# Optimization experiments

Hardware: AMD Instinct MI355X
Metric: run time of the kernel (lower is better)

## Reference

```python
import jax, jax.numpy as jnp
import numpy as np

B, N = 4, 512
D_MODEL, ATOM_CH = 256, 5
PAIR_H, N_RBF, RBF_MAX = 128, 16, 4.0
LN_EPS = 1e-5


def setup_inputs() -> dict:
    key = jax.random.key(0)
    ks = jax.random.split(key, 12)
    sd = 1.0 / np.sqrt(D_MODEL)
    sh = 1.0 / np.sqrt(PAIR_H)
    return {
        "trunk_out": jax.random.normal(ks[0], (B, N, D_MODEL), jnp.float32),
        "coords": jax.random.normal(ks[1], (B, N, 3), jnp.float32),
        "pad_mask": jax.random.randint(ks[2], (B, N), 0, 2).astype(bool),
        "ln_g": jnp.ones((D_MODEL,), jnp.float32),
        "ln_b": jnp.zeros((D_MODEL,), jnp.float32),
        "w_a1": jax.random.normal(ks[3], (D_MODEL, D_MODEL), jnp.float32) * sd,
        "b_a1": jnp.zeros((D_MODEL,), jnp.float32),
        "w_a2": jax.random.normal(ks[4], (D_MODEL, ATOM_CH), jnp.float32) * sd,
        "b_a2": jnp.zeros((ATOM_CH,), jnp.float32),
        "w_pi": jax.random.normal(ks[5], (D_MODEL, PAIR_H), jnp.float32) * sd,
        "w_pj": jax.random.normal(ks[6], (D_MODEL, PAIR_H), jnp.float32) * sd,
        "w_pr": jax.random.normal(ks[7], (N_RBF, PAIR_H), jnp.float32) * 0.25,
        "b_p1": jnp.zeros((PAIR_H,), jnp.float32),
        "w_p2": jax.random.normal(ks[8], (PAIR_H,), jnp.float32) * sh,
        "b_p2": jnp.zeros((1,), jnp.float32),
    }


def _forward(trunk_out, coords, pad_mask, ln_g, ln_b, w_a1, b_a1, w_a2, b_a2,
             w_pi, w_pj, w_pr, b_p1, w_p2, b_p2):
    dt = trunk_out.dtype
    valid = ~pad_mask                                   # (B, N)
    validf = valid.astype(dt)

    # ---- atom head: LayerNorm -> Linear -> SiLU -> Linear, pad-masked ----
    mu = trunk_out.mean(-1, keepdims=True)
    var = jnp.mean((trunk_out - mu) ** 2, -1, keepdims=True)
    xn = (trunk_out - mu) * jax.lax.rsqrt(var + LN_EPS) * ln_g + ln_b
    atom_delta = jax.nn.silu(xn @ w_a1 + b_a1) @ w_a2 + b_a2
    atom_delta = jnp.where(pad_mask[..., None], jnp.zeros((), dt), atom_delta)

    # ---- geometry features (non-periodic adapter) ----
    delta = coords[:, :, None, :] - coords[:, None, :, :]   # (B, N, N, 3)
    sq = jnp.sum(delta * delta, -1)
    dist = jnp.sqrt(jnp.maximum(sq, 1e-12))                 # safe sqrt (diag)
    centers = jnp.linspace(0.0, RBF_MAX, N_RBF, dtype=dt)
    gamma = jnp.asarray(1.0 / (RBF_MAX / max(N_RBF - 1, 1)) ** 2, dt)
    rbf = jnp.exp(-gamma * (dist[..., None] - centers) ** 2)  # (B, N, N, R)
    pair_mask = valid[:, :, None] & valid[:, None, :]

    # ---- pair head: LazyLinear on cat([hi, hj, rbf]) == sum of 3 projections ----
    pi = jnp.einsum('bid,dh->bih', trunk_out, w_pi)         # (B, N, H)
    pj = jnp.einsum('bjd,dh->bjh', trunk_out, w_pj)
    h1 = jax.nn.silu(pi[:, :, None, :] + pj[:, None, :, :]
                     + jnp.einsum('bijr,rh->bijh', rbf, w_pr) + b_p1)
    pw = jnp.einsum('bijh,h->bij', h1, w_p2) + b_p2[0]      # (B, N, N)
    pw = jnp.where(pair_mask, pw, jnp.zeros((), dt))
    pw = jnp.where(jnp.eye(N, dtype=bool), jnp.zeros((), dt), pw)  # zero diag

    # ---- weighted-sum coordinate update ----
    coord_delta = jnp.einsum('bij,bijc->bic', pw, delta)    # (B, N, 3)
    denom = jnp.maximum(validf.sum(1, keepdims=True), 1.0)  # (B, 1)
    coord_delta = coord_delta / denom[..., None]
    coord_delta = jnp.where(pad_mask[..., None], jnp.zeros((), dt), coord_delta)
    mean = (coord_delta * validf[..., None]).sum(1, keepdims=True) / denom[..., None]
    coord_delta = jnp.where(pad_mask[..., None], jnp.zeros((), dt), coord_delta - mean)
    return atom_delta, coord_delta


def reference(trunk_out, coords, pad_mask, ln_g, ln_b, w_a1, b_a1, w_a2, b_a2,
              w_pi, w_pj, w_pr, b_p1, w_p2, b_p2):
    return _forward(trunk_out, coords, pad_mask, ln_g, ln_b, w_a1, b_a1,
                    w_a2, b_a2, w_pi, w_pj, w_pr, b_p1, w_p2, b_p2)
```

## Files before the change

kernel.cpp:

```cpp
#include <hip/hip_runtime.h>
#include <hip/hip_bf16.h>

#define BN 2048
#define NSEQ 512
#define D 256
#define H 128
#define R 16
#define AC 5
#define CHUNK 128
#define ROWG 4
#define SPLIT 4

using bf16 = __hip_bfloat16;

__device__ __forceinline__ float fast_silu(float t) {
    const float e = __expf(-t);
    return t * __builtin_amdgcn_rcpf(1.0f + e);
}
__device__ __forceinline__ float bf2f(unsigned short u) {
    return __uint_as_float(((unsigned)u) << 16);
}

__global__ __launch_bounds__(256) void batch_kernel(
    const int* __restrict__ pad, int* __restrict__ jlist_g, int* __restrict__ M_g)
{
    const int b = blockIdx.x;
    const int tid = threadIdx.x;
    __shared__ int s_wcnt[8];
    __shared__ int s_wbase[8];
    const int wv = tid >> 6, lane = tid & 63;
    unsigned long long bm[2];
    #pragma unroll
    for (int cc = 0; cc < 2; ++cc) {
        const int j = cc * 256 + tid;
        const int ok = (pad[b * NSEQ + j] == 0);
        bm[cc] = __ballot(ok);
        if (lane == 0) s_wcnt[cc * 4 + wv] = __popcll(bm[cc]);
    }
    __syncthreads();
    if (tid == 0) {
        int acc = 0;
        #pragma unroll
        for (int q = 0; q < 8; ++q) { s_wbase[q] = acc; acc += s_wcnt[q]; }
        M_g[b] = acc;
    }
    __syncthreads();
    #pragma unroll
    for (int cc = 0; cc < 2; ++cc) {
        const int j = cc * 256 + tid;
        if (pad[b * NSEQ + j] == 0) {
            const int pos = s_wbase[cc * 4 + wv]
                          + __popcll(bm[cc] & ((1ull << lane) - 1ull));
            jlist_g[b * NSEQ + pos] = j;
        }
    }
}

__global__ __launch_bounds__(256) void row_kernel(
    const float* __restrict__ trunk, const int* __restrict__ pad,
    const float* __restrict__ ln_g, const float* __restrict__ ln_b,
    const float* __restrict__ w_a1, const float* __restrict__ b_a1,
    const float* __restrict__ w_a2, const float* __restrict__ b_a2,
    const float* __restrict__ w_pi, const float* __restrict__ w_pj,
    const float* __restrict__ b_p1,
    float* __restrict__ out_atom, float* __restrict__ pj_o,
    unsigned short* __restrict__ pib_o)
{
    const int row0 = blockIdx.x * ROWG;
    const int tid = threadIdx.x;
    const int wv = tid >> 6, lane = tid & 63;
    __shared__ __align__(16) float x_t[D][ROWG];
    __shared__ __align__(16) float xn_t[D][ROWG];
    __shared__ float y[ROWG][D];
    __shared__ float mu_s[ROWG], rs_s[ROWG];

    #pragma unroll
    for (int g = 0; g < ROWG; ++g)
        x_t[tid][g] = trunk[(size_t)(row0 + g) * D + tid];
    __syncthreads();

    {
        const int g = wv;
        float s = 0.0f, ss = 0.0f;
        #pragma unroll
        for (int e = lane; e < D; e += 64) {
            const float v = x_t[e][g];
            s += v; ss += v * v;
        }
        #pragma unroll
        for (int off = 32; off; off >>= 1) {
            s  += __shfl_xor(s, off);
            ss += __shfl_xor(ss, off);
        }
        if (lane == 0) {
            const float mu  = s * (1.0f / D);
            const float var = ss * (1.0f / D) - mu * mu;
            mu_s[g] = mu;
            rs_s[g] = rsqrtf(var + 1e-5f);
        }
    }
    __syncthreads();
    {
        const float lg = ln_g[tid], lb = ln_b[tid];
        #pragma unroll
        for (int g = 0; g < ROWG; ++g)
            xn_t[tid][g] = (x_t[tid][g] - mu_s[g]) * rs_s[g] * lg + lb;
    }
    __syncthreads();

    {
        float acc0 = b_a1[tid], acc1 = acc0, acc2 = acc0, acc3 = acc0;
        for (int d = 0; d < D; ++d) {
            const float w = w_a1[d * D + tid];
            const float4 xv = *(const float4*)xn_t[d];
            acc0 = fmaf(xv.x, w, acc0);
            acc1 = fmaf(xv.y, w, acc1);
            acc2 = fmaf(xv.z, w, acc2);
            acc3 = fmaf(xv.w, w, acc3);
        }
        y[0][tid] = acc0 / (1.0f + expf(-acc0));
        y[1][tid] = acc1 / (1.0f + expf(-acc1));
        y[2][tid] = acc2 / (1.0f + expf(-acc2));
        y[3][tid] = acc3 / (1.0f + expf(-acc3));
    }

    float p0 = 0.0f, p1 = 0.0f, p2 = 0.0f, p3 = 0.0f;
    if (tid < H) {
        for (int d = 0; d < D; ++d) {
            const float w = w_pi[d * H + tid];
            const float4 xv = *(const float4*)x_t[d];
            p0 = fmaf(xv.x, w, p0);
            p1 = fmaf(xv.y, w, p1);
            p2 = fmaf(xv.z, w, p2);
            p3 = fmaf(xv.w, w, p3);
        }
        const float bb = b_p1[tid];
        p0 += bb; p1 += bb; p2 += bb; p3 += bb;
    } else {
        const int h = tid - H;
        for (int d = 0; d < D; ++d) {
            const float w = w_pj[d * H + h];
            const float4 xv = *(const float4*)x_t[d];
            p0 = fmaf(xv.x, w, p0);
            p1 = fmaf(xv.y, w, p1);
            p2 = fmaf(xv.z, w, p2);
            p3 = fmaf(xv.w, w, p3);
        }
    }
    __syncthreads();
    if (tid < H) {
        const float pv[ROWG] = {p0, p1, p2, p3};
        #pragma unroll
        for (int g = 0; g < ROWG; ++g) {
            const bf16 pb = __float2bfloat16(pv[g]);
            pib_o[(size_t)(row0 + g) * H + tid] = *(const unsigned short*)&pb;
        }
    } else {
        const int h = tid - H;
        const float pv[ROWG] = {p0, p1, p2, p3};
        #pragma unroll
        for (int g = 0; g < ROWG; ++g)
            pj_o[(size_t)(row0 + g) * H + h] = pv[g];
    }

    if (tid < ROWG * AC) {
        const int g = tid / AC, c = tid % AC;
        float a = b_a2[c];
        for (int d = 0; d < D; ++d) a = fmaf(y[g][d], w_a2[d * AC + c], a);
        out_atom[(row0 + g) * AC + c] = (pad[row0 + g] != 0) ? 0.0f : a;
    }
}

__device__ __forceinline__ void pair_body(
    const float pvx, const float pvy,
    const float* __restrict__ rbf_row, const float4 dk,
    const float pibx, const float piby,
    const float* wprA, const float* wprB, const float2 wp22,
    float& cdx, float& cdy, float& cdz,
    float& sdx, float& sdy, float& sdz)
{
    float t0a = pibx + pvx, t0b = 0.0f;
    float t1a = piby + pvy, t1b = 0.0f;
    #pragma unroll
    for (int r = 0; r < R; r += 2) {
        const float qa = rbf_row[r];
        const float qb = rbf_row[r + 1];
        t0a = fmaf(qa, wprA[r],     t0a);
        t0b = fmaf(qb, wprA[r + 1], t0b);
        t1a = fmaf(qa, wprB[r],     t1a);
        t1b = fmaf(qb, wprB[r + 1], t1b);
    }
    const float u0 = fast_silu(t0a + t0b);
    const float u1 = fast_silu(t1a + t1b);
    const float part = u0 * wp22.x + u1 * wp22.y;
    cdx = fmaf(part, dk.x, cdx);
    cdy = fmaf(part, dk.y, cdy);
    cdz = fmaf(part, dk.z, cdz);
    sdx += dk.x; sdy += dk.y; sdz += dk.z;
}

__global__ __launch_bounds__(256) void pair_kernel(
    const float* __restrict__ coords, const int* __restrict__ pad,
    const float* __restrict__ w_pr, const float* __restrict__ w_p2,
    const float* __restrict__ b_p2,
    const float* __restrict__ pj_i, const unsigned short* __restrict__ pib_i,
    const int* __restrict__ jlist_g, const int* __restrict__ M_g,
    float* __restrict__ cd_part)
{
    const int row  = blockIdx.x >> 2;
    const int part_id = blockIdx.x & 3;
    const int b = row >> 9;
    const int tid = threadIdx.x;

    if (pad[row] != 0) {
        if (tid == 0) {
            cd_part[(row * SPLIT + part_id) * 3 + 0] = 0.0f;
            cd_part[(row * SPLIT + part_id) * 3 + 1] = 0.0f;
            cd_part[(row * SPLIT + part_id) * 3 + 2] = 0.0f;
        }
        return;
    }

    __shared__ __align__(16) float s_rbf[CHUNK][20];
    __shared__ __align__(16) float4 s_d4[CHUNK];
    __shared__ int   s_jl[CHUNK];
    __shared__ float rw1[4], rw2[4], rw3[4];

    const int wv = tid >> 6, lane = tid & 63;
    const int M = M_g[b];
    const int Mq  = (M + SPLIT - 1) / SPLIT;
    const int kLo = part_id * Mq;
    const int kHi = min(M, kLo + Mq);

    float wprA[R], wprB[R];
    #pragma unroll
    for (int r = 0; r < R; ++r) {
        const float2 wv2 = ((const float2*)(w_pr + r * H))[lane];
        wprA[r] = wv2.x;
        wprB[r] = wv2.y;
    }
    const ushort2 pibu = ((const ushort2*)(pib_i + (size_t)row * H))[lane];
    const float pibx = bf2f(pibu.x), piby = bf2f(pibu.y);
    const float2 wp22 = ((const float2*)w_p2)[lane];
    const float bp2 = b_p2[0];
    const float cix = coords[(size_t)row * 3 + 0];
    const float ciy = coords[(size_t)row * 3 + 1];
    const float ciz = coords[(size_t)row * 3 + 2];

    float cdx = 0.0f, cdy = 0.0f, cdz = 0.0f;
    float sdx = 0.0f, sdy = 0.0f, sdz = 0.0f;
    const float* pjb = pj_i + (size_t)b * NSEQ * H;
    const float gamma = 14.0625f;

    for (int c0 = kLo; c0 < kHi; c0 += CHUNK) {
        const int cn = (kHi - c0 < CHUNK) ? (kHi - c0) : CHUNK;
        __syncthreads();
        if (tid < cn) {
            const int j = jlist_g[b * NSEQ + c0 + tid];
            s_jl[tid] = j;
            const float* cj = coords + (size_t)(b * NSEQ + j) * 3;
            const float dx = cix - cj[0];
            const float dy = ciy - cj[1];
            const float dz = ciz - cj[2];
            const float sq = dx * dx + dy * dy + dz * dz;
            const float dist = sqrtf(fmaxf(sq, 1e-12f));
            s_d4[tid] = make_float4(dx, dy, dz, 0.0f);
            #pragma unroll
            for (int c = 0; c < 4; ++c) {
                float4 q;
                const float t0 = dist - (float)(4.0 * (4 * c + 0) / 15.0);
                const float t1 = dist - (float)(4.0 * (4 * c + 1) / 15.0);
                const float t2 = dist - (float)(4.0 * (4 * c + 2) / 15.0);
                const float t3 = dist - (float)(4.0 * (4 * c + 3) / 15.0);
                q.x = __expf(-gamma * t0 * t0);
                q.y = __expf(-gamma * t1 * t1);
                q.z = __expf(-gamma * t2 * t2);
                q.w = __expf(-gamma * t3 * t3);
                *(float4*)(&s_rbf[tid][4 * c]) = q;
            }
        }
        __syncthreads();
        for (int k = wv; k < cn; k += 16) {
            const int k1 = k + 4, k2 = k + 8, k3 = k + 12;
            const bool h1 = (k1 < cn), h2 = (k2 < cn), h3 = (k3 < cn);
            const int j0 = s_jl[k];
            const int j1 = s_jl[h1 ? k1 : k];
            const int j2 = s_jl[h2 ? k2 : k];
            const int j3 = s_jl[h3 ? k3 : k];
            const float2 pv0 = ((const float2*)(pjb + (size_t)j0 * H))[lane];
            const float2 pv1 = ((const float2*)(pjb + (size_t)j1 * H))[lane];
            const float2 pv2 = ((const float2*)(pjb + (size_t)j2 * H))[lane];
            const float2 pv3 = ((const float2*)(pjb + (size_t)j3 * H))[lane];

            pair_body(pv0.x, pv0.y, s_rbf[k], s_d4[k], pibx, piby,
                      wprA, wprB, wp22, cdx, cdy, cdz, sdx, sdy, sdz);
            if (h1) pair_body(pv1.x, pv1.y, s_rbf[k1], s_d4[k1], pibx, piby,
                              wprA, wprB, wp22, cdx, cdy, cdz, sdx, sdy, sdz);
            if (h2) pair_body(pv2.x, pv2.y, s_rbf[k2], s_d4[k2], pibx, piby,
                              wprA, wprB, wp22, cdx, cdy, cdz, sdx, sdy, sdz);
            if (h3) pair_body(pv3.x, pv3.y, s_rbf[k3], s_d4[k3], pibx, piby,
                              wprA, wprB, wp22, cdx, cdy, cdz, sdx, sdy, sdz);
        }
    }
    #pragma unroll
    for (int off = 32; off; off >>= 1) {
        cdx += __shfl_xor(cdx, off);
        cdy += __shfl_xor(cdy, off);
        cdz += __shfl_xor(cdz, off);
    }
    if (lane == 0) {
        rw1[wv] = cdx + bp2 * sdx;
        rw2[wv] = cdy + bp2 * sdy;
        rw3[wv] = cdz + bp2 * sdz;
    }
    __syncthreads();
    if (tid == 0) {
        cd_part[(row * SPLIT + part_id) * 3 + 0] = rw1[0] + rw1[1] + rw1[2] + rw1[3];
        cd_part[(row * SPLIT + part_id) * 3 + 1] = rw2[0] + rw2[1] + rw2[2] + rw2[3];
        cd_part[(row * SPLIT + part_id) * 3 + 2] = rw3[0] + rw3[1] + rw3[2] + rw3[3];
    }
}

__global__ __launch_bounds__(256) void finalize_kernel(
    const float* __restrict__ cd_part, const int* __restrict__ pad,
    float* __restrict__ out_coord)
{
    const int b = blockIdx.x;
    const int tid = threadIdx.x;
    __shared__ float r1[256], r2[256], r3[256], r4[256];
    float sx = 0.0f, sy = 0.0f, sz = 0.0f, cnt = 0.0f;
    for (int ii = tid; ii < NSEQ; ii += 256) {
        const int row = b * NSEQ + ii;
        if (pad[row] == 0) {
            float cx = 0.0f, cy = 0.0f, cz = 0.0f;
            #pragma unroll
            for (int q = 0; q < SPLIT; ++q) {
                cx += cd_part[(row * SPLIT + q) * 3 + 0];
                cy += cd_part[(row * SPLIT + q) * 3 + 1];
                cz += cd_part[(row * SPLIT + q) * 3 + 2];
            }
            sx += cx; sy += cy; sz += cz;
            cnt += 1.0f;
        }
    }
    r1[tid] = sx; r2[tid] = sy; r3[tid] = sz; r4[tid] = cnt;
    __syncthreads();
    for (int s = 128; s > 0; s >>= 1) {
        if (tid < s) {
            r1[tid] += r1[tid + s]; r2[tid] += r2[tid + s];
            r3[tid] += r3[tid + s]; r4[tid] += r4[tid + s];
        }
        __syncthreads();
    }
    const float denom = fmaxf(r4[0], 1.0f);
    const float inv_d = 1.0f / denom;
    const float mx = r1[0] * inv_d * inv_d;
    const float my = r2[0] * inv_d * inv_d;
    const float mz = r3[0] * inv_d * inv_d;
    for (int ii = tid; ii < NSEQ; ii += 256) {
        const int row = b * NSEQ + ii;
        const bool v = (pad[row] == 0);
        float cx = 0.0f, cy = 0.0f, cz = 0.0f;
        #pragma unroll
        for (int q = 0; q < SPLIT; ++q) {
            cx += cd_part[(row * SPLIT + q) * 3 + 0];
            cy += cd_part[(row * SPLIT + q) * 3 + 1];
            cz += cd_part[(row * SPLIT + q) * 3 + 2];
        }
        out_coord[row * 3 + 0] = v ? cx * inv_d - mx : 0.0f;
        out_coord[row * 3 + 1] = v ? cy * inv_d - my : 0.0f;
        out_coord[row * 3 + 2] = v ? cz * inv_d - mz : 0.0f;
    }
}

extern "C" void kernel_launch(void* const* d_in, const int* in_sizes, int n_in,
                              void* d_out, int out_size, void* d_ws, size_t ws_size,
                              hipStream_t stream) {
    const float* trunk  = (const float*)d_in[0];
    const float* coords = (const float*)d_in[1];
    const int*   pad    = (const int*)d_in[2];
    const float* ln_g   = (const float*)d_in[3];
    const float* ln_b   = (const float*)d_in[4];
    const float* w_a1   = (const float*)d_in[5];
    const float* b_a1   = (const float*)d_in[6];
    const float* w_a2   = (const float*)d_in[7];
    const float* b_a2   = (const float*)d_in[8];
    const float* w_pi   = (const float*)d_in[9];
    const float* w_pj   = (const float*)d_in[10];
    const float* w_pr   = (const float*)d_in[11];
    const float* b_p1   = (const float*)d_in[12];
    const float* w_p2   = (const float*)d_in[13];
    const float* b_p2   = (const float*)d_in[14];

    float* out_atom  = (float*)d_out;
    float* out_coord = out_atom + (size_t)BN * AC;

    int*   jlist_g = (int*)d_ws;
    int*   M_g     = jlist_g + 4 * NSEQ;
    float* cd_part = (float*)(M_g + 16);
    float* pj_buf  = cd_part + (size_t)BN * SPLIT * 3;
    unsigned short* pib_buf = (unsigned short*)(pj_buf + (size_t)BN * H);

    batch_kernel<<<4, 256, 0, stream>>>(pad, jlist_g, M_g);
    row_kernel<<<BN / ROWG, 256, 0, stream>>>(trunk, pad, ln_g, ln_b, w_a1, b_a1,
                                              w_a2, b_a2, w_pi, w_pj, b_p1,
                                              out_atom, pj_buf, pib_buf);
    pair_kernel<<<BN * SPLIT, 256, 0, stream>>>(coords, pad, w_pr, w_p2, b_p2,
                                                pj_buf, pib_buf, jlist_g, M_g, cd_part);
    finalize_kernel<<<4, 256, 0, stream>>>(cd_part, pad, out_coord);
}
```

Measured before the change: 69.63 us.

## Block pair kernel over compacted i-rows to reuse pj loads across rows

```diff
diff --git a/kernel.cpp b/kernel.cpp
--- a/kernel.cpp
+++ b/kernel.cpp
@@ -7,9 +7,10 @@
 #define H 128
 #define R 16
 #define AC 5
-#define CHUNK 128
 #define ROWG 4
-#define SPLIT 4
+#define IG 4
+#define JSPLIT 8
+#define JCHUNK 32
 
 using bf16 = __hip_bfloat16;
 
@@ -200,37 +201,58 @@
 }
 
 __global__ __launch_bounds__(256) void pair_kernel(
-    const float* __restrict__ coords, const int* __restrict__ pad,
+    const float* __restrict__ coords,
     const float* __restrict__ w_pr, const float* __restrict__ w_p2,
     const float* __restrict__ b_p2,
     const float* __restrict__ pj_i, const unsigned short* __restrict__ pib_i,
     const int* __restrict__ jlist_g, const int* __restrict__ M_g,
     float* __restrict__ cd_part)
 {
-    const int row  = blockIdx.x >> 2;
-    const int part_id = blockIdx.x & 3;
-    const int b = row >> 9;
-    const int tid = threadIdx.x;
-
-    if (pad[row] != 0) {
-        if (tid == 0) {
-            cd_part[(row * SPLIT + part_id) * 3 + 0] = 0.0f;
-            cd_part[(row * SPLIT + part_id) * 3 + 1] = 0.0f;
-            cd_part[(row * SPLIT + part_id) * 3 + 2] = 0.0f;
+    const int part = blockIdx.x & (JSPLIT - 1);
+    const int tmp  = blockIdx.x >> 3;
+    const int gi   = tmp & ((NSEQ / IG) - 1);
+    const int b    = tmp >> 7;
+    const int tid  = threadIdx.x;
+    const int wv = tid >> 6, lane = tid & 63;
+
+    const int M  = M_g[b];
+    const int i0 = gi * IG;
+    if (i0 >= M) return;
+    const int nI = min(IG, M - i0);
+
+    const int Mq  = (M + JSPLIT - 1) >> 3;
+    const int kLo = part * Mq;
+    const int kHi = min(M, kLo + Mq);
+
+    __shared__ int   s_irow[IG];
+    __shared__ float s_ci[IG][3];
+    __shared__ __align__(16) float s_rbf[IG][JCHUNK][20];
+    __shared__ __align__(16) float4 s_d4[IG][JCHUNK];
+    __shared__ int   s_jl[JCHUNK];
+    __shared__ float s_red[4][IG][3];
+
+    if (tid < IG) {
+        if (tid < nI) {
+            const int il  = jlist_g[b * NSEQ + i0 + tid];
+            const int row = b * NSEQ + il;
+            s_irow[tid] = row;
+            s_ci[tid][0] = coords[(size_t)row * 3 + 0];
+            s_ci[tid][1] = coords[(size_t)row * 3 + 1];
+            s_ci[tid][2] = coords[(size_t)row * 3 + 2];
+        } else {
+            s_irow[tid] = b * NSEQ;
+            s_ci[tid][0] = 0.0f; s_ci[tid][1] = 0.0f; s_ci[tid][2] = 0.0f;
+        }
+    }
+    __syncthreads();
+
+    if (kLo >= kHi) {
+        if (tid < nI * 3) {
+            const int ii = tid / 3, c = tid % 3;
+            cd_part[((size_t)s_irow[ii] * JSPLIT + part) * 3 + c] = 0.0f;
         }
         return;
     }
-
-    __shared__ __align__(16) float s_rbf[CHUNK][20];
-    __shared__ __align__(16) float4 s_d4[CHUNK];
-    __shared__ int   s_jl[CHUNK];
-    __shared__ float rw1[4], rw2[4], rw3[4];
-
-    const int wv = tid >> 6, lane = tid & 63;
-    const int M = M_g[b];
-    const int Mq  = (M + SPLIT - 1) / SPLIT;
-    const int kLo = part_id * Mq;
-    const int kHi = min(M, kLo + Mq);
 
     float wprA[R], wprB[R];
     #pragma unroll
@@ -239,85 +261,90 @@
         wprA[r] = wv2.x;
         wprB[r] = wv2.y;
     }
-    const ushort2 pibu = ((const ushort2*)(pib_i + (size_t)row * H))[lane];
-    const float pibx = bf2f(pibu.x), piby = bf2f(pibu.y);
+    float pibx[IG], piby[IG];
+    #pragma unroll
+    for (int ii = 0; ii < IG; ++ii) {
+        const ushort2 u = ((const ushort2*)(pib_i + (size_t)s_irow[ii] * H))[lane];
+        pibx[ii] = bf2f(u.x);
+        piby[ii] = bf2f(u.y);
+    }
     const float2 wp22 = ((const float2*)w_p2)[lane];
     const float bp2 = b_p2[0];
-    const float cix = coords[(size_t)row * 3 + 0];
-    const float ciy = coords[(size_t)row * 3 + 1];
-    const float ciz = coords[(size_t)row * 3 + 2];
-
-    float cdx = 0.0f, cdy = 0.0f, cdz = 0.0f;
-    float sdx = 0.0f, sdy = 0.0f, sdz = 0.0f;
+
+    float cdx[IG] = {0.f, 0.f, 0.f, 0.f};
+    float cdy[IG] = {0.f, 0.f, 0.f, 0.f};
+    float cdz[IG] = {0.f, 0.f, 0.f, 0.f};
+    float sdx[IG] = {0.f, 0.f, 0.f, 0.f};
+    float sdy[IG] = {0.f, 0.f, 0.f, 0.f};
+    float sdz[IG] = {0.f, 0.f, 0.f, 0.f};
     const float* pjb = pj_i + (size_t)b * NSEQ * H;
     const float gamma = 14.0625f;
 
-    for (int c0 = kLo; c0 < kHi; c0 += CHUNK) {
-        const int cn = (kHi - c0 < CHUNK) ? (kHi - c0) : CHUNK;
+    for (int c0 = kLo; c0 < kHi; c0 += JCHUNK) {
+        const int cn = min(JCHUNK, kHi - c0);
         __syncthreads();
-        if (tid < cn) {
-            const int j = jlist_g[b * NSEQ + c0 + tid];
-            s_jl[tid] = j;
-            const float* cj = coords + (size_t)(b * NSEQ + j) * 3;
-            const float dx = cix - cj[0];
-            const float dy = ciy - cj[1];
-            const float dz = ciz - cj[2];
-            const float sq = dx * dx + dy * dy + dz * dz;
-            const float dist = sqrtf(fmaxf(sq, 1e-12f));
-            s_d4[tid] = make_float4(dx, dy, dz, 0.0f);
+        {
+            const int kk = tid & (JCHUNK - 1);
+            const int ii = tid >> 5;
+            if (ii < IG && kk < cn) {
+                const int j = jlist_g[b * NSEQ + c0 + kk];
+                if (ii == 0) s_jl[kk] = j;
+                const float* cj = coords + (size_t)(b * NSEQ + j) * 3;
+                const float dx = s_ci[ii][0] - cj[0];
+                const float dy = s_ci[ii][1] - cj[1];
+                const float dz = s_ci[ii][2] - cj[2];
+                const float sq = dx * dx + dy * dy + dz * dz;
+                const float dist = sqrtf(fmaxf(sq, 1e-12f));
+                s_d4[ii][kk] = make_float4(dx, dy, dz, 0.0f);
+                #pragma unroll
+                for (int c = 0; c < 4; ++c) {
+                    float4 q;
+                    const float t0 = dist - (float)(4.0 * (4 * c + 0) / 15.0);
+                    const float t1 = dist - (float)(4.0 * (4 * c + 1) / 15.0);
+                    const float t2 = dist - (float)(4.0 * (4 * c + 2) / 15.0);
+                    const float t3 = dist - (float)(4.0 * (4 * c + 3) / 15.0);
+                    q.x = __expf(-gamma * t0 * t0);
+                    q.y = __expf(-gamma * t1 * t1);
+                    q.z = __expf(-gamma * t2 * t2);
+                    q.w = __expf(-gamma * t3 * t3);
+                    *(float4*)(&s_rbf[ii][kk][4 * c]) = q;
+                }
+            }
+        }
+        __syncthreads();
+        for (int k = wv; k < cn; k += 4) {
+            const int j = s_jl[k];
+            const float2 pv = ((const float2*)(pjb + (size_t)j * H))[lane];
             #pragma unroll
-            for (int c = 0; c < 4; ++c) {
-                float4 q;
-                const float t0 = dist - (float)(4.0 * (4 * c + 0) / 15.0);
-                const float t1 = dist - (float)(4.0 * (4 * c + 1) / 15.0);
-                const float t2 = dist - (float)(4.0 * (4 * c + 2) / 15.0);
-                const float t3 = dist - (float)(4.0 * (4 * c + 3) / 15.0);
-                q.x = __expf(-gamma * t0 * t0);
-                q.y = __expf(-gamma * t1 * t1);
-                q.z = __expf(-gamma * t2 * t2);
-                q.w = __expf(-gamma * t3 * t3);
-                *(float4*)(&s_rbf[tid][4 * c]) = q;
+            for (int ii = 0; ii < IG; ++ii) {
+                pair_body(pv.x, pv.y, s_rbf[ii][k], s_d4[ii][k],
+                          pibx[ii], piby[ii], wprA, wprB, wp22,
+                          cdx[ii], cdy[ii], cdz[ii], sdx[ii], sdy[ii], sdz[ii]);
             }
         }
-        __syncthreads();
-        for (int k = wv; k < cn; k += 16) {
-            const int k1 = k + 4, k2 = k + 8, k3 = k + 12;
-            const bool h1 = (k1 < cn), h2 = (k2 < cn), h3 = (k3 < cn);
-            const int j0 = s_jl[k];
-            const int j1 = s_jl[h1 ? k1 : k];
-            const int j2 = s_jl[h2 ? k2 : k];
-            const int j3 = s_jl[h3 ? k3 : k];
-            const float2 pv0 = ((const float2*)(pjb + (size_t)j0 * H))[lane];
-            const float2 pv1 = ((const float2*)(pjb + (size_t)j1 * H))[lane];
-            const float2 pv2 = ((const float2*)(pjb + (size_t)j2 * H))[lane];
-            const float2 pv3 = ((const float2*)(pjb + (size_t)j3 * H))[lane];
-
-            pair_body(pv0.x, pv0.y, s_rbf[k], s_d4[k], pibx, piby,
-                      wprA, wprB, wp22, cdx, cdy, cdz, sdx, sdy, sdz);
-            if (h1) pair_body(pv1.x, pv1.y, s_rbf[k1], s_d4[k1], pibx, piby,
-                              wprA, wprB, wp22, cdx, cdy, cdz, sdx, sdy, sdz);
-            if (h2) pair_body(pv2.x, pv2.y, s_rbf[k2], s_d4[k2], pibx, piby,
-                              wprA, wprB, wp22, cdx, cdy, cdz, sdx, sdy, sdz);
-            if (h3) pair_body(pv3.x, pv3.y, s_rbf[k3], s_d4[k3], pibx, piby,
-                              wprA, wprB, wp22, cdx, cdy, cdz, sdx, sdy, sdz);
-        }
-    }
-    #pragma unroll
-    for (int off = 32; off; off >>= 1) {
-        cdx += __shfl_xor(cdx, off);
-        cdy += __shfl_xor(cdy, off);
-        cdz += __shfl_xor(cdz, off);
+    }
+    #pragma unroll
+    for (int ii = 0; ii < IG; ++ii) {
+        #pragma unroll
+        for (int off = 32; off; off >>= 1) {
+            cdx[ii] += __shfl_xor(cdx[ii], off);
+            cdy[ii] += __shfl_xor(cdy[ii], off);
+            cdz[ii] += __shfl_xor(cdz[ii], off);
+        }
     }
     if (lane == 0) {
-        rw1[wv] = cdx + bp2 * sdx;
-        rw2[wv] = cdy + bp2 * sdy;
-        rw3[wv] = cdz + bp2 * sdz;
-    }
-    __syncthreads();
-    if (tid == 0) {
-        cd_part[(row * SPLIT + part_id) * 3 + 0] = rw1[0] + rw1[1] + rw1[2] + rw1[3];
-        cd_part[(row * SPLIT + part_id) * 3 + 1] = rw2[0] + rw2[1] + rw2[2] + rw2[3];
-        cd_part[(row * SPLIT + part_id) * 3 + 2] = rw3[0] + rw3[1] + rw3[2] + rw3[3];
+        #pragma unroll
+        for (int ii = 0; ii < IG; ++ii) {
+            s_red[wv][ii][0] = cdx[ii] + bp2 * sdx[ii];
+            s_red[wv][ii][1] = cdy[ii] + bp2 * sdy[ii];
+            s_red[wv][ii][2] = cdz[ii] + bp2 * sdz[ii];
+        }
+    }
+    __syncthreads();
+    if (tid < nI * 3) {
+        const int ii = tid / 3, c = tid % 3;
+        cd_part[((size_t)s_irow[ii] * JSPLIT + part) * 3 + c] =
+            s_red[0][ii][c] + s_red[1][ii][c] + s_red[2][ii][c] + s_red[3][ii][c];
     }
 }
 
@@ -334,10 +361,10 @@
         if (pad[row] == 0) {
             float cx = 0.0f, cy = 0.0f, cz = 0.0f;
             #pragma unroll
-            for (int q = 0; q < SPLIT; ++q) {
-                cx += cd_part[(row * SPLIT + q) * 3 + 0];
-                cy += cd_part[(row * SPLIT + q) * 3 + 1];
-                cz += cd_part[(row * SPLIT + q) * 3 + 2];
+            for (int q = 0; q < JSPLIT; ++q) {
+                cx += cd_part[((size_t)row * JSPLIT + q) * 3 + 0];
+                cy += cd_part[((size_t)row * JSPLIT + q) * 3 + 1];
+                cz += cd_part[((size_t)row * JSPLIT + q) * 3 + 2];
             }
             sx += cx; sy += cy; sz += cz;
             cnt += 1.0f;
@@ -359,17 +386,22 @@
     const float mz = r3[0] * inv_d * inv_d;
     for (int ii = tid; ii < NSEQ; ii += 256) {
         const int row = b * NSEQ + ii;
-        const bool v = (pad[row] == 0);
-        float cx = 0.0f, cy = 0.0f, cz = 0.0f;
-        #pragma unroll
-        for (int q = 0; q < SPLIT; ++q) {
-            cx += cd_part[(row * SPLIT + q) * 3 + 0];
-            cy += cd_part[(row * SPLIT + q) * 3 + 1];
-            cz += cd_part[(row * SPLIT + q) * 3 + 2];
-        }
-        out_coord[row * 3 + 0] = v ? cx * inv_d - mx : 0.0f;
-        out_coord[row * 3 + 1] = v ? cy * inv_d - my : 0.0f;
-        out_coord[row * 3 + 2] = v ? cz * inv_d - mz : 0.0f;
+        if (pad[row] == 0) {
+            float cx = 0.0f, cy = 0.0f, cz = 0.0f;
+            #pragma unroll
+            for (int q = 0; q < JSPLIT; ++q) {
+                cx += cd_part[((size_t)row * JSPLIT + q) * 3 + 0];
+                cy += cd_part[((size_t)row * JSPLIT + q) * 3 + 1];
+                cz += cd_part[((size_t)row * JSPLIT + q) * 3 + 2];
+            }
+            out_coord[row * 3 + 0] = cx * inv_d - mx;
+            out_coord[row * 3 + 1] = cy * inv_d - my;
+            out_coord[row * 3 + 2] = cz * inv_d - mz;
+        } else {
+            out_coord[row * 3 + 0] = 0.0f;
+            out_coord[row * 3 + 1] = 0.0f;
+            out_coord[row * 3 + 2] = 0.0f;
+        }
     }
 }
 
@@ -398,14 +430,14 @@
     int*   jlist_g = (int*)d_ws;
     int*   M_g     = jlist_g + 4 * NSEQ;
     float* cd_part = (float*)(M_g + 16);
-    float* pj_buf  = cd_part + (size_t)BN * SPLIT * 3;
+    float* pj_buf  = cd_part + (size_t)BN * JSPLIT * 3;
     unsigned short* pib_buf = (unsigned short*)(pj_buf + (size_t)BN * H);
 
     batch_kernel<<<4, 256, 0, stream>>>(pad, jlist_g, M_g);
     row_kernel<<<BN / ROWG, 256, 0, stream>>>(trunk, pad, ln_g, ln_b, w_a1, b_a1,
                                               w_a2, b_a2, w_pi, w_pj, b_p1,
                                               out_atom, pj_buf, pib_buf);
-    pair_kernel<<<BN * SPLIT, 256, 0, stream>>>(coords, pad, w_pr, w_p2, b_p2,
-                                                pj_buf, pib_buf, jlist_g, M_g, cd_part);
+    pair_kernel<<<4 * (NSEQ / IG) * JSPLIT, 256, 0, stream>>>(
+        coords, w_pr, w_p2, b_p2, pj_buf, pib_buf, jlist_g, M_g, cd_part);
     finalize_kernel<<<4, 256, 0, stream>>>(cd_part, pad, out_coord);
 }
```

Result: slower. 79.48 us (+14.1%).

## Process eight rows per row-kernel block with 512 threads and split GEMM roles

Applied to the files above, without the earlier changes.

```diff
diff --git a/kernel.cpp b/kernel.cpp
--- a/kernel.cpp
+++ b/kernel.cpp
@@ -8,7 +8,7 @@
 #define R 16
 #define AC 5
 #define CHUNK 128
-#define ROWG 4
+#define ROWG 8
 #define SPLIT 4
 
 using bf16 = __hip_bfloat16;
@@ -56,7 +56,7 @@
     }
 }
 
-__global__ __launch_bounds__(256) void row_kernel(
+__global__ __launch_bounds__(512) void row_kernel(
     const float* __restrict__ trunk, const int* __restrict__ pad,
     const float* __restrict__ ln_g, const float* __restrict__ ln_b,
     const float* __restrict__ w_a1, const float* __restrict__ b_a1,
@@ -69,22 +69,25 @@
     const int row0 = blockIdx.x * ROWG;
     const int tid = threadIdx.x;
     const int wv = tid >> 6, lane = tid & 63;
-    __shared__ __align__(16) float x_t[D][ROWG];
-    __shared__ __align__(16) float xn_t[D][ROWG];
+    __shared__ __align__(16) float x_t[2][D][4];
+    __shared__ __align__(16) float xn_t[2][D][4];
     __shared__ float y[ROWG][D];
     __shared__ float mu_s[ROWG], rs_s[ROWG];
 
     #pragma unroll
-    for (int g = 0; g < ROWG; ++g)
-        x_t[tid][g] = trunk[(size_t)(row0 + g) * D + tid];
+    for (int gg = 0; gg < 4; ++gg) {
+        const int g = gg * 2 + (tid >> 8);
+        const int e = tid & 255;
+        x_t[g >> 2][e][g & 3] = trunk[(size_t)(row0 + g) * D + e];
+    }
     __syncthreads();
 
     {
         const int g = wv;
         float s = 0.0f, ss = 0.0f;
         #pragma unroll
-        for (int e = lane; e < D; e += 64) {
-            const float v = x_t[e][g];
+        for (int e2 = lane; e2 < D; e2 += 64) {
+            const float v = x_t[g >> 2][e2][g & 3];
             s += v; ss += v * v;
         }
         #pragma unroll
@@ -100,68 +103,73 @@
         }
     }
     __syncthreads();
-    {
-        const float lg = ln_g[tid], lb = ln_b[tid];
-        #pragma unroll
-        for (int g = 0; g < ROWG; ++g)
-            xn_t[tid][g] = (x_t[tid][g] - mu_s[g]) * rs_s[g] * lg + lb;
-    }
-    __syncthreads();
-
-    {
-        float acc0 = b_a1[tid], acc1 = acc0, acc2 = acc0, acc3 = acc0;
+    #pragma unroll
+    for (int gg = 0; gg < 4; ++gg) {
+        const int g = gg * 2 + (tid >> 8);
+        const int e = tid & 255;
+        xn_t[g >> 2][e][g & 3] =
+            (x_t[g >> 2][e][g & 3] - mu_s[g]) * rs_s[g] * ln_g[e] + ln_b[e];
+    }
+    __syncthreads();
+
+    if (tid < 256) {
+        const float bb = b_a1[tid];
+        float a0 = bb, a1v = bb, a2v = bb, a3 = bb, a4 = bb, a5 = bb, a6 = bb, a7 = bb;
         for (int d = 0; d < D; ++d) {
             const float w = w_a1[d * D + tid];
-            const float4 xv = *(const float4*)xn_t[d];
-            acc0 = fmaf(xv.x, w, acc0);
-            acc1 = fmaf(xv.y, w, acc1);
-            acc2 = fmaf(xv.z, w, acc2);
-            acc3 = fmaf(xv.w, w, acc3);
-        }
-        y[0][tid] = acc0 / (1.0f + expf(-acc0));
-        y[1][tid] = acc1 / (1.0f + expf(-acc1));
-        y[2][tid] = acc2 / (1.0f + expf(-acc2));
-        y[3][tid] = acc3 / (1.0f + expf(-acc3));
-    }
-
-    float p0 = 0.0f, p1 = 0.0f, p2 = 0.0f, p3 = 0.0f;
-    if (tid < H) {
+            const float4 lo = *(const float4*)xn_t[0][d];
+            const float4 hi = *(const float4*)xn_t[1][d];
+            a0  = fmaf(lo.x, w, a0);  a1v = fmaf(lo.y, w, a1v);
+            a2v = fmaf(lo.z, w, a2v); a3  = fmaf(lo.w, w, a3);
+            a4  = fmaf(hi.x, w, a4);  a5  = fmaf(hi.y, w, a5);
+            a6  = fmaf(hi.z, w, a6);  a7  = fmaf(hi.w, w, a7);
+        }
+        y[0][tid] = a0  / (1.0f + expf(-a0));
+        y[1][tid] = a1v / (1.0f + expf(-a1v));
+        y[2][tid] = a2v / (1.0f + expf(-a2v));
+        y[3][tid] = a3  / (1.0f + expf(-a3));
+        y[4][tid] = a4  / (1.0f + expf(-a4));
+        y[5][tid] = a5  / (1.0f + expf(-a5));
+        y[6][tid] = a6  / (1.0f + expf(-a6));
+        y[7][tid] = a7  / (1.0f + expf(-a7));
+    } else if (tid < 384) {
+        const int h = tid - 256;
+        float p0 = 0.f, p1 = 0.f, p2 = 0.f, p3 = 0.f, p4 = 0.f, p5 = 0.f, p6 = 0.f, p7 = 0.f;
         for (int d = 0; d < D; ++d) {
-            const float w = w_pi[d * H + tid];
-            const float4 xv = *(const float4*)x_t[d];
-            p0 = fmaf(xv.x, w, p0);
-            p1 = fmaf(xv.y, w, p1);
-            p2 = fmaf(xv.z, w, p2);
-            p3 = fmaf(xv.w, w, p3);
-        }
-        const float bb = b_p1[tid];
-        p0 += bb; p1 += bb; p2 += bb; p3 += bb;
+            const float w = w_pi[d * H + h];
+            const float4 lo = *(const float4*)x_t[0][d];
+            const float4 hi = *(const float4*)x_t[1][d];
+            p0 = fmaf(lo.x, w, p0); p1 = fmaf(lo.y, w, p1);
+            p2 = fmaf(lo.z, w, p2); p3 = fmaf(lo.w, w, p3);
+            p4 = fmaf(hi.x, w, p4); p5 = fmaf(hi.y, w, p5);
+            p6 = fmaf(hi.z, w, p6); p7 = fmaf(hi.w, w, p7);
+        }
+        const float bb = b_p1[h];
+        const float pv[ROWG] = {p0 + bb, p1 + bb, p2 + bb, p3 + bb,
+                                p4 + bb, p5 + bb, p6 + bb, p7 + bb};
+        #pragma unroll
+        for (int g = 0; g < ROWG; ++g) {
+            const bf16 pb = __float2bfloat16(pv[g]);
+            pib_o[(size_t)(row0 + g) * H + h] = *(const unsigned short*)&pb;
+        }
     } else {
-        const int h = tid - H;
+        const int h = tid - 384;
+        float p0 = 0.f, p1 = 0.f, p2 = 0.f, p3 = 0.f, p4 = 0.f, p5 = 0.f, p6 = 0.f, p7 = 0.f;
         for (int d = 0; d < D; ++d) {
             const float w = w_pj[d * H + h];
-            const float4 xv = *(const float4*)x_t[d];
-            p0 = fmaf(xv.x, w, p0);
-            p1 = fmaf(xv.y, w, p1);
-            p2 = fmaf(xv.z, w, p2);
-            p3 = fmaf(xv.w, w, p3);
-        }
-    }
-    __syncthreads();
-    if (tid < H) {
-        const float pv[ROWG] = {p0, p1, p2, p3};
-        #pragma unroll
-        for (int g = 0; g < ROWG; ++g) {
-            const bf16 pb = __float2bfloat16(pv[g]);
-            pib_o[(size_t)(row0 + g) * H + tid] = *(const unsigned short*)&pb;
-        }
-    } else {
-        const int h = tid - H;
-        const float pv[ROWG] = {p0, p1, p2, p3};
+            const float4 lo = *(const float4*)x_t[0][d];
+            const float4 hi = *(const float4*)x_t[1][d];
+            p0 = fmaf(lo.x, w, p0); p1 = fmaf(lo.y, w, p1);
+            p2 = fmaf(lo.z, w, p2); p3 = fmaf(lo.w, w, p3);
+            p4 = fmaf(hi.x, w, p4); p5 = fmaf(hi.y, w, p5);
+            p6 = fmaf(hi.z, w, p6); p7 = fmaf(hi.w, w, p7);
+        }
+        const float pv[ROWG] = {p0, p1, p2, p3, p4, p5, p6, p7};
         #pragma unroll
         for (int g = 0; g < ROWG; ++g)
             pj_o[(size_t)(row0 + g) * H + h] = pv[g];
     }
+    __syncthreads();
 
     if (tid < ROWG * AC) {
         const int g = tid / AC, c = tid % AC;
@@ -402,7 +410,7 @@
     unsigned short* pib_buf = (unsigned short*)(pj_buf + (size_t)BN * H);
 
     batch_kernel<<<4, 256, 0, stream>>>(pad, jlist_g, M_g);
-    row_kernel<<<BN / ROWG, 256, 0, stream>>>(trunk, pad, ln_g, ln_b, w_a1, b_a1,
+    row_kernel<<<BN / ROWG, 512, 0, stream>>>(trunk, pad, ln_g, ln_b, w_a1, b_a1,
                                               w_a2, b_a2, w_pi, w_pj, b_p1,
                                               out_atom, pj_buf, pib_buf);
     pair_kernel<<<BN * SPLIT, 256, 0, stream>>>(coords, pad, w_pr, w_p2, b_p2,
```

Result: no change. 68.97 us (-0.9%).
